# Kernel optimization log

Hardware: AMD Instinct MI355X
Metric: run time of the kernel (lower is better)

The kernel has to match this reference:

```python
import jax, jax.numpy as jnp
import numpy as np

B, T, E, H = 64, 512, 256, 128


def setup_inputs() -> dict:
    key = jax.random.key(0)
    ks = jax.random.split(key, 7)
    s = 1.0 / np.sqrt(H)  # PyTorch LSTM default init range
    inputs = jax.random.normal(ks[0], (B, T, E), jnp.float32)
    labels = jax.random.randint(ks[1], (B, T), 0, H)
    W_ih = jax.random.uniform(ks[2], (4 * H, E), jnp.float32, -s, s)
    W_hh = jax.random.uniform(ks[3], (4 * H, H), jnp.float32, -s, s)
    b_ih = jax.random.uniform(ks[4], (4 * H,), jnp.float32, -s, s)
    b_hh = jax.random.uniform(ks[5], (4 * H,), jnp.float32, -s, s)
    transition = jax.random.uniform(ks[6], (H, H), jnp.float32)  # torch.rand
    return {"inputs": inputs, "labels": labels, "W_ih": W_ih, "W_hh": W_hh,
            "b_ih": b_ih, "b_hh": b_hh, "transition": transition}


def _lstm(x, W_ih, W_hh, b_ih, b_hh):
    # x: (T, B, E) -> hs: (T, B, H). PyTorch gate order: i, f, g, o.
    Bn = x.shape[1]
    Hn = W_hh.shape[1]

    def step(carry, xt):
        h, c = carry
        g = xt @ W_ih.T + b_ih + h @ W_hh.T + b_hh  # (B, 4H)
        i, f, gg, o = jnp.split(g, 4, axis=-1)
        c = jax.nn.sigmoid(f) * c + jax.nn.sigmoid(i) * jnp.tanh(gg)
        h = jax.nn.sigmoid(o) * jnp.tanh(c)
        return (h, c), h

    h0 = jnp.zeros((Bn, Hn), x.dtype)
    (_, _), hs = jax.lax.scan(step, (h0, h0), x)
    return hs


def reference(inputs, labels, W_ih, W_hh, b_ih, b_hh, transition):
    x = inputs.transpose(1, 0, 2)  # (T, B, E)
    trans = jax.nn.softmax(transition, axis=1)  # row-softmax transition
    hs = _lstm(x, W_ih, W_hh, b_ih, b_hh)  # (T, B, H)
    Hbth = jax.nn.softmax(hs, axis=2).transpose(1, 0, 2)  # (B, T, H)

    # gold-path score Pr: emissions at gold tags + transition scores
    emit = jnp.take_along_axis(Hbth, labels[:, :, None], axis=2)[..., 0].sum(axis=1)  # (B,)
    tr_score = trans[labels[:, :-1], labels[:, 1:]].sum(axis=1)  # (B,)
    Pr = emit + tr_score

    # CRF forward algorithm (partition score Ps) via scan over time
    pre0 = Hbth[:, 0, :] + trans[0]  # (B, H)

    def crf_step(pre, h_t):
        # Z[b, i, j] = pre[b, i] + trans[i, j] + h_t[b, j]
        Z = pre[:, :, None] + trans[None] + h_t[:, None, :]
        return jax.nn.logsumexp(Z, axis=1), None

    pre, _ = jax.lax.scan(crf_step, pre0, Hbth[:, 1:, :].transpose(1, 0, 2))
    Ps = jax.nn.logsumexp(pre + trans[-1][None, :], axis=1)  # (B,)

    return (Ps - Pr).sum()
```

## Files before the change

### kernel.cpp

```cpp
#include <hip/hip_runtime.h>
#include <hip/hip_bf16.h>
#include <cstdint>

#define BB 64
#define TT 512
#define EE 256
#define HH 128
#define G4 512

typedef _Float16 half2_t __attribute__((ext_vector_type(2)));
typedef _Float16 f16x4 __attribute__((ext_vector_type(4)));
typedef _Float16 f16x8 __attribute__((ext_vector_type(8)));
typedef float f32x4 __attribute__((ext_vector_type(4)));

#define BC(x) __builtin_bit_cast(half2_t, x)

__device__ __forceinline__ float fdot2f(half2_t a, half2_t b, float c) {
#if defined(__has_builtin)
#if __has_builtin(__builtin_amdgcn_fdot2)
  return __builtin_amdgcn_fdot2(a, b, c, false);
#else
  return c + (float)a[0] * (float)b[0] + (float)a[1] * (float)b[1];
#endif
#else
  return c + (float)a[0] * (float)b[0] + (float)a[1] * (float)b[1];
#endif
}

__device__ __forceinline__ float rcp_(float x) { return __builtin_amdgcn_rcpf(x); }
__device__ __forceinline__ float tanh_(float x) {
  float ax = fabsf(x);
  float e = __expf(-2.f * ax);
  float r = (1.f - e) * rcp_(1.f + e);
  return copysignf(r, x);
}

__device__ __forceinline__ float readlane_f(float x, int lane) {
#if defined(__has_builtin)
#if __has_builtin(__builtin_amdgcn_readlane)
  return __builtin_bit_cast(float, __builtin_amdgcn_readlane(__builtin_bit_cast(int, x), lane));
#else
  return __shfl(x, lane);
#endif
#else
  return __shfl(x, lane);
#endif
}

#if defined(__has_builtin)
#if __has_builtin(__builtin_amdgcn_update_dpp)
#define HAVE_DPP 1
#endif
#endif

__device__ __forceinline__ float wave_sum64_bcast(float x) {
#ifdef HAVE_DPP
#define DPP_ADD(ctrl)                                                          \
  {                                                                            \
    int _t = __builtin_amdgcn_update_dpp(0, __builtin_bit_cast(int, x), ctrl,  \
                                         0xf, 0xf, true);                      \
    x += __builtin_bit_cast(float, _t);                                        \
  }
  DPP_ADD(0x111)
  DPP_ADD(0x112)
  DPP_ADD(0x114)
  DPP_ADD(0x118)
  DPP_ADD(0x142)
  DPP_ADD(0x143)
#undef DPP_ADD
  return readlane_f(x, 63);
#else
#pragma unroll
  for (int s = 1; s <= 32; s <<= 1) x += __shfl_xor(x, s);
  return x;
#endif
}

__global__ __launch_bounds__(128) void prep_kernel(
    const float* __restrict__ transition, const float* __restrict__ W_ih,
    float* __restrict__ trans, _Float16* __restrict__ W16) {
  const int bid = blockIdx.x, t = threadIdx.x;
  if (bid < 128) {
    __shared__ float red[2];
    float v = transition[bid * HH + t];
    float m = v;
#pragma unroll
    for (int s = 32; s >= 1; s >>= 1) m = fmaxf(m, __shfl_xor(m, s));
    if ((t & 63) == 0) red[t >> 6] = m;
    __syncthreads();
    m = fmaxf(red[0], red[1]);
    float e = __expf(v - m);
    float s = e;
#pragma unroll
    for (int k = 32; k >= 1; k >>= 1) s += __shfl_xor(s, k);
    __syncthreads();
    if ((t & 63) == 0) red[t >> 6] = s;
    __syncthreads();
    trans[bid * HH + t] = e * rcp_(red[0] + red[1]);
  } else {
    const int base = (bid - 128) * 1024 + t * 8;
    float4 v0 = *(const float4*)(W_ih + base);
    float4 v1 = *(const float4*)(W_ih + base + 4);
    f16x8 h;
    h[0] = (_Float16)v0.x; h[1] = (_Float16)v0.y;
    h[2] = (_Float16)v0.z; h[3] = (_Float16)v0.w;
    h[4] = (_Float16)v1.x; h[5] = (_Float16)v1.y;
    h[6] = (_Float16)v1.z; h[7] = (_Float16)v1.w;
    *(f16x8*)(W16 + base) = h;
  }
}

__global__ __launch_bounds__(256) void gemm_in(
    const float* __restrict__ A, const _Float16* __restrict__ W16,
    const float* __restrict__ b_ih, const float* __restrict__ b_hh,
    float* __restrict__ out) {
  __shared__ _Float16 As[64][264];
  const int t = threadIdx.x;
  const int m0 = blockIdx.x * 64;
  const int n0 = blockIdx.y * 256;
  {
    const int c4 = t & 63, r0 = t >> 6;
#pragma unroll
    for (int p = 0; p < 16; ++p) {
      const int row = r0 + 4 * p;
      float4 v = *(const float4*)(A + (size_t)(m0 + row) * EE + c4 * 4);
      f16x4 h;
      h[0] = (_Float16)v.x; h[1] = (_Float16)v.y;
      h[2] = (_Float16)v.z; h[3] = (_Float16)v.w;
      *(f16x4*)&As[row][c4 * 4] = h;
    }
  }
  __syncthreads();
  const int w = t >> 6, L = t & 63;
  const int lrow = L & 15, quad = L >> 4, lk = quad * 8;
  f32x4 acc[4][4] = {};
  const _Float16* Wbase = W16 + (size_t)(n0 + w * 64) * EE;
#pragma unroll
  for (int kc = 0; kc < 8; ++kc) {
    f16x8 a[4], bf[4];
#pragma unroll
    for (int mf = 0; mf < 4; ++mf)
      a[mf] = *(const f16x8*)&As[mf * 16 + lrow][kc * 32 + lk];
#pragma unroll
    for (int nf = 0; nf < 4; ++nf)
      bf[nf] = *(const f16x8*)(Wbase + (size_t)(nf * 16 + lrow) * EE + kc * 32 + lk);
#pragma unroll
    for (int mf = 0; mf < 4; ++mf)
#pragma unroll
      for (int nf = 0; nf < 4; ++nf)
        acc[mf][nf] = __builtin_amdgcn_mfma_f32_16x16x32_f16(a[mf], bf[nf], acc[mf][nf], 0, 0, 0);
  }
#pragma unroll
  for (int nf = 0; nf < 4; ++nf) {
    const int j = n0 + w * 64 + nf * 16 + lrow;
    const float bias = b_ih[j] + b_hh[j];
#pragma unroll
    for (int mf = 0; mf < 4; ++mf) {
#pragma unroll
      for (int r = 0; r < 4; ++r) {
        const int m = m0 + mf * 16 + quad * 4 + r;
        out[(size_t)m * G4 + j] = acc[mf][nf][r] + bias;
      }
    }
  }
}

__global__ __launch_bounds__(512, 2) void lstm_crf(
    const float* __restrict__ precomp, const float* __restrict__ Whh,
    const float* __restrict__ trans, const int* __restrict__ labels,
    float* __restrict__ out_b) {
  const int b = blockIdx.x, t = threadIdx.x;
  const int g = t >> 7;
  const int j = t & 127;

  __shared__ __align__(16) _Float16 h_lds[HH];
  __shared__ __align__(16) _Float16 E_lds[HH];
  __shared__ __align__(16) float act2[G4];
  __shared__ __align__(16) float Spart2[G4];
  __shared__ int lab[TT];

  half2_t w[64];
  {
    const float4* wr = (const float4*)(Whh + (size_t)t * HH);
#pragma unroll
    for (int i = 0; i < 32; ++i) {
      float4 v = wr[i];
      half2_t p0, p1;
      p0[0] = (_Float16)v.x; p0[1] = (_Float16)v.y;
      p1[0] = (_Float16)v.z; p1[1] = (_Float16)v.w;
      w[2 * i] = p0; w[2 * i + 1] = p1;
    }
  }
  half2_t et[16];
#pragma unroll
  for (int a = 0; a < 16; ++a) {
    float e0 = __expf(trans[(g * 32 + 2 * a) * HH + j]);
    float e1 = __expf(trans[(g * 32 + 2 * a + 1) * HH + j]);
    half2_t h2; h2[0] = (_Float16)e0; h2[1] = (_Float16)e1;
    et[a] = h2;
  }
  lab[t] = labels[b * TT + t];
  if (t < HH) { h_lds[t] = (_Float16)0.f; E_lds[t] = (_Float16)0.f; }

  float tr0x = 0.f, tr0y = 0.f, tr127x = 0.f, tr127y = 0.f;
  if (t < 64) {
    float2 v0 = *(const float2*)(trans + 2 * t);
    float2 v1 = *(const float2*)(trans + 127 * HH + 2 * t);
    tr0x = v0.x; tr0y = v0.y; tr127x = v1.x; tr127y = v1.y;
  }
  float c0 = 0.f, c1 = 0.f, preA = 0.f, preB = 0.f, mused = 0.f, emit = 0.f;

  const float* pcb = precomp + (size_t)b * TT * G4 + t;
  float cbuf[8], nbuf[8];
#pragma unroll
  for (int k = 0; k < 8; ++k) cbuf[k] = pcb[(size_t)k * G4];
  __syncthreads();

#pragma unroll 1
  for (int base = 0; base < TT; base += 8) {
    const bool more = (base + 8 < TT);
    if (more) {
#pragma unroll
      for (int k = 0; k < 8; ++k) nbuf[k] = pcb[(size_t)(base + 8 + k) * G4];
    }
#pragma unroll
    for (int k = 0; k < 8; ++k) {
      const int step = base + k;
      const float cur = cbuf[k];
      float a0 = 0.f, a1 = 0.f, a2 = 0.f, a3 = 0.f;
      const float4* hv4 = (const float4*)h_lds;
#pragma unroll
      for (int kc = 0; kc < 16; ++kc) {
        float4 hb = hv4[kc];
        a0 = fdot2f(w[4 * kc + 0], BC(hb.x), a0);
        a1 = fdot2f(w[4 * kc + 1], BC(hb.y), a1);
        a2 = fdot2f(w[4 * kc + 2], BC(hb.z), a2);
        a3 = fdot2f(w[4 * kc + 3], BC(hb.w), a3);
      }
      float s0 = 0.f, s1 = 0.f;
      const float4* ev4 = (const float4*)E_lds + g * 4;
#pragma unroll
      for (int ec = 0; ec < 4; ++ec) {
        float4 eb = ev4[ec];
        s0 = fdot2f(et[4 * ec + 0], BC(eb.x), s0);
        s1 = fdot2f(et[4 * ec + 1], BC(eb.y), s1);
        s0 = fdot2f(et[4 * ec + 2], BC(eb.z), s0);
        s1 = fdot2f(et[4 * ec + 3], BC(eb.w), s1);
      }
      const float gate = cur + ((a0 + a1) + (a2 + a3));
      const bool isg = (g == 2);
      const float yy = isg ? (-2.f * fabsf(gate)) : (-gate);
      const float exv = __expf(yy);
      const float num = isg ? (1.f - exv) : 1.f;
      float av = num * rcp_(1.f + exv);
      av = isg ? copysignf(av, gate) : av;
      act2[j * 4 + g] = av;
      Spart2[j * 4 + g] = s0 + s1;
      __syncthreads();
      if (t < 64) {
        const float4* av4 = (const float4*)act2;
        float4 A0 = av4[2 * t], A1 = av4[2 * t + 1];
        const float4* sv4 = (const float4*)Spart2;
        float4 S0v = sv4[2 * t], S1v = sv4[2 * t + 1];
        c0 = A0.y * c0 + A0.x * A0.z;
        c1 = A1.y * c1 + A1.x * A1.z;
        const float h0 = A0.w * tanh_(c0), h1 = A1.w * tanh_(c1);
        const float e0 = __expf(h0), e1 = __expf(h1);
        const float denom = wave_sum64_bcast(e0 + e1);
        const float rinv = rcp_(denom);
        const float p0 = e0 * rinv, p1 = e1 * rinv;
        const float Sa = (S0v.x + S0v.y) + (S0v.z + S0v.w);
        const float Sb = (S1v.x + S1v.y) + (S1v.z + S1v.w);
        const float lgSa = __logf(Sa), lgSb = __logf(Sb);
        const float lgS0 = readlane_f(lgSa, 0);
        const int lb = lab[step];
        const float Mnext = (step == 0) ? 0.f : (mused + lgS0);
        preA = p0 + ((step == 0) ? tr0x : (mused + lgSa));
        preB = p1 + ((step == 0) ? tr0y : (mused + lgSb));
        if (2 * t == lb) emit += p0;
        if (2 * t + 1 == lb) emit += p1;
        half2_t Eh;
        Eh[0] = (_Float16)__expf(preA - Mnext);
        Eh[1] = (_Float16)__expf(preB - Mnext);
        *(half2_t*)&E_lds[2 * t] = Eh;
        half2_t Hh;
        Hh[0] = (_Float16)h0; Hh[1] = (_Float16)h1;
        *(half2_t*)&h_lds[2 * t] = Hh;
        mused = Mnext;
      }
      __syncthreads();
    }
    if (more) {
#pragma unroll
      for (int k = 0; k < 8; ++k) cbuf[k] = nbuf[k];
    }
  }
  if (t < 64) {
    float v0 = preA + tr127x, v1 = preB + tr127y;
    float m = fmaxf(v0, v1);
#pragma unroll
    for (int s = 1; s <= 32; s <<= 1) m = fmaxf(m, __shfl_xor(m, s));
    float ex = __expf(v0 - m) + __expf(v1 - m);
    float em = emit;
#pragma unroll
    for (int s = 1; s <= 32; s <<= 1) {
      ex += __shfl_xor(ex, s);
      em += __shfl_xor(em, s);
    }
    if (t == 0) out_b[b] = m + __logf(ex) - em;
  }
}

__global__ __launch_bounds__(512) void finalize_kernel(
    const float* __restrict__ trans, const int* __restrict__ labels,
    const float* __restrict__ out_b, float* __restrict__ d_out) {
  const int t = threadIdx.x;
  float a = 0.f;
  if (t < TT - 1) {
    for (int b = 0; b < BB; ++b) {
      const int l0 = labels[b * TT + t];
      const int l1 = labels[b * TT + t + 1];
      a += trans[l0 * HH + l1];
    }
  }
  float x = ((t < BB) ? out_b[t] : 0.f) - a;
  __shared__ float red[8];
#pragma unroll
  for (int s = 32; s >= 1; s >>= 1) x += __shfl_xor(x, s);
  if ((t & 63) == 0) red[t >> 6] = x;
  __syncthreads();
  if (t == 0) {
    float s = 0.f;
#pragma unroll
    for (int i = 0; i < 8; ++i) s += red[i];
    d_out[0] = s;
  }
}

extern "C" void kernel_launch(void* const* d_in, const int* in_sizes, int n_in,
                              void* d_out, int out_size, void* d_ws, size_t ws_size,
                              hipStream_t stream) {
  const float* inputs = (const float*)d_in[0];
  const int* labels = (const int*)d_in[1];
  const float* W_ih = (const float*)d_in[2];
  const float* W_hh = (const float*)d_in[3];
  const float* b_ih = (const float*)d_in[4];
  const float* b_hh = (const float*)d_in[5];
  const float* transition = (const float*)d_in[6];

  char* ws = (char*)d_ws;
  float* precomp = (float*)ws;
  float* trans = (float*)(ws + 67108864);
  _Float16* W16 = (_Float16*)(ws + 67108864 + 65536);
  float* out_b = (float*)(ws + 67108864 + 65536 + 262144);

  prep_kernel<<<256, 128, 0, stream>>>(transition, W_ih, trans, W16);
  gemm_in<<<dim3(512, 2), 256, 0, stream>>>(inputs, W16, b_ih, b_hh, precomp);
  lstm_crf<<<64, 512, 0, stream>>>(precomp, W_hh, trans, labels, out_b);
  finalize_kernel<<<1, 512, 0, stream>>>(trans, labels, out_b, (float*)d_out);
}
```

Before: 605.5 us.

## Halve recurrent block to 256 threads, each computing two gate rows

The sequential LSTM+CRF kernel now launches 256 threads per batch element instead of 512. Each thread holds two W_hh rows and two transition column slices in registers and computes two gates per step. Gate rows t and t+256 pair a sigmoid gate with either the tanh (g) gate or the o gate, and the act/Spart LDS layout changes to match. The aim is to make each per-step __syncthreads barrier cheaper with fewer waves, at the cost of doubling per-thread register use and serial ALU work per step.

New measurement: 620.8 us. +2.5%, slower.

```diff
diff --git a/kernel.cpp b/kernel.cpp
--- a/kernel.cpp
+++ b/kernel.cpp
@@ -165,41 +165,52 @@
   }
 }
 
-__global__ __launch_bounds__(512, 2) void lstm_crf(
+__global__ __launch_bounds__(256) void lstm_crf(
     const float* __restrict__ precomp, const float* __restrict__ Whh,
     const float* __restrict__ trans, const int* __restrict__ labels,
     float* __restrict__ out_b) {
   const int b = blockIdx.x, t = threadIdx.x;
-  const int g = t >> 7;
+  const int g0 = t >> 7;
   const int j = t & 127;
 
   __shared__ __align__(16) _Float16 h_lds[HH];
   __shared__ __align__(16) _Float16 E_lds[HH];
-  __shared__ __align__(16) float act2[G4];
-  __shared__ __align__(16) float Spart2[G4];
+  __shared__ __align__(16) float act[G4];
+  __shared__ __align__(16) float Spart[G4];
   __shared__ int lab[TT];
 
-  half2_t w[64];
+  half2_t w0[64], w1[64];
   {
-    const float4* wr = (const float4*)(Whh + (size_t)t * HH);
+    const float4* wr0 = (const float4*)(Whh + (size_t)t * HH);
+    const float4* wr1 = (const float4*)(Whh + (size_t)(t + 256) * HH);
 #pragma unroll
     for (int i = 0; i < 32; ++i) {
-      float4 v = wr[i];
+      float4 v = wr0[i];
       half2_t p0, p1;
       p0[0] = (_Float16)v.x; p0[1] = (_Float16)v.y;
       p1[0] = (_Float16)v.z; p1[1] = (_Float16)v.w;
-      w[2 * i] = p0; w[2 * i + 1] = p1;
-    }
-  }
-  half2_t et[16];
+      w0[2 * i] = p0; w0[2 * i + 1] = p1;
+      float4 u = wr1[i];
+      half2_t q0, q1;
+      q0[0] = (_Float16)u.x; q0[1] = (_Float16)u.y;
+      q1[0] = (_Float16)u.z; q1[1] = (_Float16)u.w;
+      w1[2 * i] = q0; w1[2 * i + 1] = q1;
+    }
+  }
+  half2_t et0[16], et1[16];
 #pragma unroll
   for (int a = 0; a < 16; ++a) {
-    float e0 = __expf(trans[(g * 32 + 2 * a) * HH + j]);
-    float e1 = __expf(trans[(g * 32 + 2 * a + 1) * HH + j]);
+    float e0 = __expf(trans[(g0 * 32 + 2 * a) * HH + j]);
+    float e1 = __expf(trans[(g0 * 32 + 2 * a + 1) * HH + j]);
     half2_t h2; h2[0] = (_Float16)e0; h2[1] = (_Float16)e1;
-    et[a] = h2;
+    et0[a] = h2;
+    float f0 = __expf(trans[((g0 + 2) * 32 + 2 * a) * HH + j]);
+    float f1 = __expf(trans[((g0 + 2) * 32 + 2 * a + 1) * HH + j]);
+    half2_t h3; h3[0] = (_Float16)f0; h3[1] = (_Float16)f1;
+    et1[a] = h3;
   }
   lab[t] = labels[b * TT + t];
+  lab[t + 256] = labels[b * TT + t + 256];
   if (t < HH) { h_lds[t] = (_Float16)0.f; E_lds[t] = (_Float16)0.f; }
 
   float tr0x = 0.f, tr0y = 0.f, tr127x = 0.f, tr127y = 0.f;
@@ -210,10 +221,14 @@
   }
   float c0 = 0.f, c1 = 0.f, preA = 0.f, preB = 0.f, mused = 0.f, emit = 0.f;
 
-  const float* pcb = precomp + (size_t)b * TT * G4 + t;
-  float cbuf[8], nbuf[8];
-#pragma unroll
-  for (int k = 0; k < 8; ++k) cbuf[k] = pcb[(size_t)k * G4];
+  const float* pc0 = precomp + (size_t)b * TT * G4 + t;
+  const float* pc1 = pc0 + 256;
+  float cb0[8], cb1[8], nb0[8], nb1[8];
+#pragma unroll
+  for (int k = 0; k < 8; ++k) {
+    cb0[k] = pc0[(size_t)k * G4];
+    cb1[k] = pc1[(size_t)k * G4];
+  }
   __syncthreads();
 
 #pragma unroll 1
@@ -221,56 +236,73 @@
     const bool more = (base + 8 < TT);
     if (more) {
 #pragma unroll
-      for (int k = 0; k < 8; ++k) nbuf[k] = pcb[(size_t)(base + 8 + k) * G4];
+      for (int k = 0; k < 8; ++k) {
+        nb0[k] = pc0[(size_t)(base + 8 + k) * G4];
+        nb1[k] = pc1[(size_t)(base + 8 + k) * G4];
+      }
     }
 #pragma unroll
     for (int k = 0; k < 8; ++k) {
       const int step = base + k;
-      const float cur = cbuf[k];
-      float a0 = 0.f, a1 = 0.f, a2 = 0.f, a3 = 0.f;
+      float a00 = 0.f, a01 = 0.f, a10 = 0.f, a11 = 0.f;
       const float4* hv4 = (const float4*)h_lds;
 #pragma unroll
       for (int kc = 0; kc < 16; ++kc) {
         float4 hb = hv4[kc];
-        a0 = fdot2f(w[4 * kc + 0], BC(hb.x), a0);
-        a1 = fdot2f(w[4 * kc + 1], BC(hb.y), a1);
-        a2 = fdot2f(w[4 * kc + 2], BC(hb.z), a2);
-        a3 = fdot2f(w[4 * kc + 3], BC(hb.w), a3);
-      }
-      float s0 = 0.f, s1 = 0.f;
-      const float4* ev4 = (const float4*)E_lds + g * 4;
+        const half2_t hx = BC(hb.x), hy = BC(hb.y), hz = BC(hb.z), hw = BC(hb.w);
+        a00 = fdot2f(w0[4 * kc + 0], hx, a00);
+        a01 = fdot2f(w0[4 * kc + 1], hy, a01);
+        a00 = fdot2f(w0[4 * kc + 2], hz, a00);
+        a01 = fdot2f(w0[4 * kc + 3], hw, a01);
+        a10 = fdot2f(w1[4 * kc + 0], hx, a10);
+        a11 = fdot2f(w1[4 * kc + 1], hy, a11);
+        a10 = fdot2f(w1[4 * kc + 2], hz, a10);
+        a11 = fdot2f(w1[4 * kc + 3], hw, a11);
+      }
+      float s00 = 0.f, s01 = 0.f, s10 = 0.f, s11 = 0.f;
+      const float4* e0v = (const float4*)E_lds + g0 * 4;
+      const float4* e1v = (const float4*)E_lds + (g0 + 2) * 4;
 #pragma unroll
       for (int ec = 0; ec < 4; ++ec) {
-        float4 eb = ev4[ec];
-        s0 = fdot2f(et[4 * ec + 0], BC(eb.x), s0);
-        s1 = fdot2f(et[4 * ec + 1], BC(eb.y), s1);
-        s0 = fdot2f(et[4 * ec + 2], BC(eb.z), s0);
-        s1 = fdot2f(et[4 * ec + 3], BC(eb.w), s1);
-      }
-      const float gate = cur + ((a0 + a1) + (a2 + a3));
-      const bool isg = (g == 2);
-      const float yy = isg ? (-2.f * fabsf(gate)) : (-gate);
+        float4 ea = e0v[ec];
+        s00 = fdot2f(et0[4 * ec + 0], BC(ea.x), s00);
+        s01 = fdot2f(et0[4 * ec + 1], BC(ea.y), s01);
+        s00 = fdot2f(et0[4 * ec + 2], BC(ea.z), s00);
+        s01 = fdot2f(et0[4 * ec + 3], BC(ea.w), s01);
+        float4 eb = e1v[ec];
+        s10 = fdot2f(et1[4 * ec + 0], BC(eb.x), s10);
+        s11 = fdot2f(et1[4 * ec + 1], BC(eb.y), s11);
+        s10 = fdot2f(et1[4 * ec + 2], BC(eb.z), s10);
+        s11 = fdot2f(et1[4 * ec + 3], BC(eb.w), s11);
+      }
+      const float gate0 = cb0[k] + (a00 + a01);
+      const float gate1 = cb1[k] + (a10 + a11);
+      const float av0 = rcp_(1.f + __expf(-gate0));
+      const bool isg = (g0 == 0);
+      const float yy = isg ? (-2.f * fabsf(gate1)) : (-gate1);
       const float exv = __expf(yy);
       const float num = isg ? (1.f - exv) : 1.f;
-      float av = num * rcp_(1.f + exv);
-      av = isg ? copysignf(av, gate) : av;
-      act2[j * 4 + g] = av;
-      Spart2[j * 4 + g] = s0 + s1;
+      float av1 = num * rcp_(1.f + exv);
+      av1 = isg ? copysignf(av1, gate1) : av1;
+      act[t] = av0;
+      act[t + 256] = av1;
+      Spart[t] = s00 + s01;
+      Spart[t + 256] = s10 + s11;
       __syncthreads();
       if (t < 64) {
-        const float4* av4 = (const float4*)act2;
-        float4 A0 = av4[2 * t], A1 = av4[2 * t + 1];
-        const float4* sv4 = (const float4*)Spart2;
-        float4 S0v = sv4[2 * t], S1v = sv4[2 * t + 1];
-        c0 = A0.y * c0 + A0.x * A0.z;
-        c1 = A1.y * c1 + A1.x * A1.z;
-        const float h0 = A0.w * tanh_(c0), h1 = A1.w * tanh_(c1);
+        const float2* a2 = (const float2*)act;
+        float2 I = a2[t], F = a2[64 + t], G = a2[128 + t], O = a2[192 + t];
+        const float2* s2 = (const float2*)Spart;
+        float2 Sq0 = s2[t], Sq1 = s2[64 + t], Sq2 = s2[128 + t], Sq3 = s2[192 + t];
+        c0 = F.x * c0 + I.x * G.x;
+        c1 = F.y * c1 + I.y * G.y;
+        const float h0 = O.x * tanh_(c0), h1 = O.y * tanh_(c1);
         const float e0 = __expf(h0), e1 = __expf(h1);
         const float denom = wave_sum64_bcast(e0 + e1);
         const float rinv = rcp_(denom);
         const float p0 = e0 * rinv, p1 = e1 * rinv;
-        const float Sa = (S0v.x + S0v.y) + (S0v.z + S0v.w);
-        const float Sb = (S1v.x + S1v.y) + (S1v.z + S1v.w);
+        const float Sa = (Sq0.x + Sq1.x) + (Sq2.x + Sq3.x);
+        const float Sb = (Sq0.y + Sq1.y) + (Sq2.y + Sq3.y);
         const float lgSa = __logf(Sa), lgSb = __logf(Sb);
         const float lgS0 = readlane_f(lgSa, 0);
         const int lb = lab[step];
@@ -292,7 +324,7 @@
     }
     if (more) {
 #pragma unroll
-      for (int k = 0; k < 8; ++k) cbuf[k] = nbuf[k];
+      for (int k = 0; k < 8; ++k) { cb0[k] = nb0[k]; cb1[k] = nb1[k]; }
     }
   }
   if (t < 64) {
@@ -356,6 +388,6 @@
 
   prep_kernel<<<256, 128, 0, stream>>>(transition, W_ih, trans, W16);
   gemm_in<<<dim3(512, 2), 256, 0, stream>>>(inputs, W16, b_ih, b_hh, precomp);
-  lstm_crf<<<64, 512, 0, stream>>>(precomp, W_hh, trans, labels, out_b);
+  lstm_crf<<<64, 256, 0, stream>>>(precomp, W_hh, trans, labels, out_b);
   finalize_kernel<<<1, 512, 0, stream>>>(trans, labels, out_b, (float*)d_out);
 }
```

## Pack two batch sequences per 1024-thread block in LSTM-CRF kernel

Applied to the files above, without the earlier changes.

Each block now processes two batch elements, with one 512-thread half per sequence, halving the grid to 32 blocks. The gate and partition LDS buffers change from an interleaved j*4+g layout to a gate-major layout read as float2. The apparent aim is to share barriers and the CU across two independent recurrences to hide latency. The 1024-thread launch bound limits registers per thread, so the per-thread weight arrays may spill. Half as many CUs are used.

Result: slower. 1.158 ms (+91.2%).

```diff
diff --git a/kernel.cpp b/kernel.cpp
--- a/kernel.cpp
+++ b/kernel.cpp
@@ -165,23 +165,26 @@
   }
 }
 
-__global__ __launch_bounds__(512, 2) void lstm_crf(
+__global__ __launch_bounds__(1024) void lstm_crf(
     const float* __restrict__ precomp, const float* __restrict__ Whh,
     const float* __restrict__ trans, const int* __restrict__ labels,
     float* __restrict__ out_b) {
-  const int b = blockIdx.x, t = threadIdx.x;
-  const int g = t >> 7;
-  const int j = t & 127;
-
-  __shared__ __align__(16) _Float16 h_lds[HH];
-  __shared__ __align__(16) _Float16 E_lds[HH];
-  __shared__ __align__(16) float act2[G4];
-  __shared__ __align__(16) float Spart2[G4];
-  __shared__ int lab[TT];
+  const int t = threadIdx.x;
+  const int cc = t >> 9;
+  const int tt = t & 511;
+  const int bb = blockIdx.x * 2 + cc;
+  const int g = tt >> 7;
+  const int j = tt & 127;
+
+  __shared__ __align__(16) _Float16 h_lds[2][HH];
+  __shared__ __align__(16) _Float16 E_lds[2][HH];
+  __shared__ __align__(16) float act[2][G4];
+  __shared__ __align__(16) float Spart[2][G4];
+  __shared__ int lab[2][TT];
 
   half2_t w[64];
   {
-    const float4* wr = (const float4*)(Whh + (size_t)t * HH);
+    const float4* wr = (const float4*)(Whh + (size_t)tt * HH);
 #pragma unroll
     for (int i = 0; i < 32; ++i) {
       float4 v = wr[i];
@@ -199,18 +202,18 @@
     half2_t h2; h2[0] = (_Float16)e0; h2[1] = (_Float16)e1;
     et[a] = h2;
   }
-  lab[t] = labels[b * TT + t];
-  if (t < HH) { h_lds[t] = (_Float16)0.f; E_lds[t] = (_Float16)0.f; }
+  lab[cc][tt] = labels[bb * TT + tt];
+  if (tt < HH) { h_lds[cc][tt] = (_Float16)0.f; E_lds[cc][tt] = (_Float16)0.f; }
 
   float tr0x = 0.f, tr0y = 0.f, tr127x = 0.f, tr127y = 0.f;
-  if (t < 64) {
-    float2 v0 = *(const float2*)(trans + 2 * t);
-    float2 v1 = *(const float2*)(trans + 127 * HH + 2 * t);
+  if (tt < 64) {
+    float2 v0 = *(const float2*)(trans + 2 * tt);
+    float2 v1 = *(const float2*)(trans + 127 * HH + 2 * tt);
     tr0x = v0.x; tr0y = v0.y; tr127x = v1.x; tr127y = v1.y;
   }
   float c0 = 0.f, c1 = 0.f, preA = 0.f, preB = 0.f, mused = 0.f, emit = 0.f;
 
-  const float* pcb = precomp + (size_t)b * TT * G4 + t;
+  const float* pcb = precomp + (size_t)bb * TT * G4 + tt;
   float cbuf[8], nbuf[8];
 #pragma unroll
   for (int k = 0; k < 8; ++k) cbuf[k] = pcb[(size_t)k * G4];
@@ -228,7 +231,7 @@
       const int step = base + k;
       const float cur = cbuf[k];
       float a0 = 0.f, a1 = 0.f, a2 = 0.f, a3 = 0.f;
-      const float4* hv4 = (const float4*)h_lds;
+      const float4* hv4 = (const float4*)h_lds[cc];
 #pragma unroll
       for (int kc = 0; kc < 16; ++kc) {
         float4 hb = hv4[kc];
@@ -238,7 +241,7 @@
         a3 = fdot2f(w[4 * kc + 3], BC(hb.w), a3);
       }
       float s0 = 0.f, s1 = 0.f;
-      const float4* ev4 = (const float4*)E_lds + g * 4;
+      const float4* ev4 = (const float4*)E_lds[cc] + g * 4;
 #pragma unroll
       for (int ec = 0; ec < 4; ++ec) {
         float4 eb = ev4[ec];
@@ -254,38 +257,38 @@
       const float num = isg ? (1.f - exv) : 1.f;
       float av = num * rcp_(1.f + exv);
       av = isg ? copysignf(av, gate) : av;
-      act2[j * 4 + g] = av;
-      Spart2[j * 4 + g] = s0 + s1;
+      act[cc][tt] = av;
+      Spart[cc][tt] = s0 + s1;
       __syncthreads();
-      if (t < 64) {
-        const float4* av4 = (const float4*)act2;
-        float4 A0 = av4[2 * t], A1 = av4[2 * t + 1];
-        const float4* sv4 = (const float4*)Spart2;
-        float4 S0v = sv4[2 * t], S1v = sv4[2 * t + 1];
-        c0 = A0.y * c0 + A0.x * A0.z;
-        c1 = A1.y * c1 + A1.x * A1.z;
-        const float h0 = A0.w * tanh_(c0), h1 = A1.w * tanh_(c1);
+      if (tt < 64) {
+        const float2* a2p = (const float2*)act[cc];
+        float2 I = a2p[tt], F = a2p[64 + tt], G = a2p[128 + tt], O = a2p[192 + tt];
+        const float2* s2p = (const float2*)Spart[cc];
+        float2 Sq0 = s2p[tt], Sq1 = s2p[64 + tt], Sq2 = s2p[128 + tt], Sq3 = s2p[192 + tt];
+        c0 = F.x * c0 + I.x * G.x;
+        c1 = F.y * c1 + I.y * G.y;
+        const float h0 = O.x * tanh_(c0), h1 = O.y * tanh_(c1);
         const float e0 = __expf(h0), e1 = __expf(h1);
         const float denom = wave_sum64_bcast(e0 + e1);
         const float rinv = rcp_(denom);
         const float p0 = e0 * rinv, p1 = e1 * rinv;
-        const float Sa = (S0v.x + S0v.y) + (S0v.z + S0v.w);
-        const float Sb = (S1v.x + S1v.y) + (S1v.z + S1v.w);
+        const float Sa = (Sq0.x + Sq1.x) + (Sq2.x + Sq3.x);
+        const float Sb = (Sq0.y + Sq1.y) + (Sq2.y + Sq3.y);
         const float lgSa = __logf(Sa), lgSb = __logf(Sb);
         const float lgS0 = readlane_f(lgSa, 0);
-        const int lb = lab[step];
+        const int lb = lab[cc][step];
         const float Mnext = (step == 0) ? 0.f : (mused + lgS0);
         preA = p0 + ((step == 0) ? tr0x : (mused + lgSa));
         preB = p1 + ((step == 0) ? tr0y : (mused + lgSb));
-        if (2 * t == lb) emit += p0;
-        if (2 * t + 1 == lb) emit += p1;
+        if (2 * tt == lb) emit += p0;
+        if (2 * tt + 1 == lb) emit += p1;
         half2_t Eh;
         Eh[0] = (_Float16)__expf(preA - Mnext);
         Eh[1] = (_Float16)__expf(preB - Mnext);
-        *(half2_t*)&E_lds[2 * t] = Eh;
+        *(half2_t*)&E_lds[cc][2 * tt] = Eh;
         half2_t Hh;
         Hh[0] = (_Float16)h0; Hh[1] = (_Float16)h1;
-        *(half2_t*)&h_lds[2 * t] = Hh;
+        *(half2_t*)&h_lds[cc][2 * tt] = Hh;
         mused = Mnext;
       }
       __syncthreads();
@@ -295,7 +298,7 @@
       for (int k = 0; k < 8; ++k) cbuf[k] = nbuf[k];
     }
   }
-  if (t < 64) {
+  if (tt < 64) {
     float v0 = preA + tr127x, v1 = preB + tr127y;
     float m = fmaxf(v0, v1);
 #pragma unroll
@@ -307,7 +310,7 @@
       ex += __shfl_xor(ex, s);
       em += __shfl_xor(em, s);
     }
-    if (t == 0) out_b[b] = m + __logf(ex) - em;
+    if (tt == 0) out_b[bb] = m + __logf(ex) - em;
   }
 }
 
@@ -356,6 +359,6 @@
 
   prep_kernel<<<256, 128, 0, stream>>>(transition, W_ih, trans, W16);
   gemm_in<<<dim3(512, 2), 256, 0, stream>>>(inputs, W16, b_ih, b_hh, precomp);
-  lstm_crf<<<64, 512, 0, stream>>>(precomp, W_hh, trans, labels, out_b);
+  lstm_crf<<<32, 1024, 0, stream>>>(precomp, W_hh, trans, labels, out_b);
   finalize_kernel<<<1, 512, 0, stream>>>(trans, labels, out_b, (float*)d_out);
 }
```

## Use MFMA for LSTM recurrent matvec with gate-interleaved weight layout

Applied to the files above, without the earlier changes.

Replaces the per-thread fdot2 recurrent matvec with 16x16x32 f16 MFMA instructions. W_hh and the precomputed input projection are permuted so the four gates of each hidden unit sit in adjacent columns, which lets the cell update be done inside the MFMA wave without the act2 LDS round-trip. The h buffer is double-buffered, barriers use a custom lgkmcnt wait, and the precomp prefetch now covers one step instead of eight. This is meant to shorten the serial per-step latency, but the matvec computes redundant columns and the launch bound drops to one block per CU.

New measurement: 579.3 us. 4.3% less time.

```diff
diff --git a/kernel.cpp b/kernel.cpp
--- a/kernel.cpp
+++ b/kernel.cpp
@@ -15,6 +15,8 @@
 
 #define BC(x) __builtin_bit_cast(half2_t, x)
 
+#define BAR() asm volatile("s_waitcnt lgkmcnt(0)\n\ts_barrier" ::: "memory")
+
 __device__ __forceinline__ float fdot2f(half2_t a, half2_t b, float c) {
 #if defined(__has_builtin)
 #if __has_builtin(__builtin_amdgcn_fdot2)
@@ -28,6 +30,7 @@
 }
 
 __device__ __forceinline__ float rcp_(float x) { return __builtin_amdgcn_rcpf(x); }
+__device__ __forceinline__ float sigmoid_(float x) { return rcp_(1.f + __expf(-x)); }
 __device__ __forceinline__ float tanh_(float x) {
   float ax = fabsf(x);
   float e = __expf(-2.f * ax);
@@ -76,6 +79,10 @@
 #endif
 }
 
+__device__ __host__ __forceinline__ int permj(int j) {
+  return ((j & 127) << 2) | (j >> 7);
+}
+
 __global__ __launch_bounds__(128) void prep_kernel(
     const float* __restrict__ transition, const float* __restrict__ W_ih,
     float* __restrict__ trans, _Float16* __restrict__ W16) {
@@ -99,6 +106,8 @@
     trans[bid * HH + t] = e * rcp_(red[0] + red[1]);
   } else {
     const int base = (bid - 128) * 1024 + t * 8;
+    const int row = base >> 8;
+    const int col = base & 255;
     float4 v0 = *(const float4*)(W_ih + base);
     float4 v1 = *(const float4*)(W_ih + base + 4);
     f16x8 h;
@@ -106,7 +115,7 @@
     h[2] = (_Float16)v0.z; h[3] = (_Float16)v0.w;
     h[4] = (_Float16)v1.x; h[5] = (_Float16)v1.y;
     h[6] = (_Float16)v1.z; h[7] = (_Float16)v1.w;
-    *(f16x8*)(W16 + base) = h;
+    *(f16x8*)(W16 + (size_t)permj(row) * EE + col) = h;
   }
 }
 
@@ -153,7 +162,8 @@
 #pragma unroll
   for (int nf = 0; nf < 4; ++nf) {
     const int j = n0 + w * 64 + nf * 16 + lrow;
-    const float bias = b_ih[j] + b_hh[j];
+    const int jo = ((j & 3) << 7) | (j >> 2);
+    const float bias = b_ih[jo] + b_hh[jo];
 #pragma unroll
     for (int mf = 0; mf < 4; ++mf) {
 #pragma unroll
@@ -165,42 +175,49 @@
   }
 }
 
-__global__ __launch_bounds__(512, 2) void lstm_crf(
+__global__ __launch_bounds__(512, 1) void lstm_crf(
     const float* __restrict__ precomp, const float* __restrict__ Whh,
     const float* __restrict__ trans, const int* __restrict__ labels,
     float* __restrict__ out_b) {
   const int b = blockIdx.x, t = threadIdx.x;
-  const int g = t >> 7;
-  const int j = t & 127;
-
-  __shared__ __align__(16) _Float16 h_lds[HH];
+  const int w = t >> 6, l = t & 63, q = l >> 4, l15 = l & 15;
+  const int c2 = l15 & 3;
+  const int g2 = t >> 7, jj = t & 127;
+
+  __shared__ __align__(16) _Float16 h_lds[2][HH];
   __shared__ __align__(16) _Float16 E_lds[HH];
-  __shared__ __align__(16) float act2[G4];
-  __shared__ __align__(16) float Spart2[G4];
+  __shared__ __align__(16) float Spart[G4];
   __shared__ int lab[TT];
 
-  half2_t w[64];
-  {
-    const float4* wr = (const float4*)(Whh + (size_t)t * HH);
-#pragma unroll
-    for (int i = 0; i < 32; ++i) {
-      float4 v = wr[i];
-      half2_t p0, p1;
-      p0[0] = (_Float16)v.x; p0[1] = (_Float16)v.y;
-      p1[0] = (_Float16)v.z; p1[1] = (_Float16)v.w;
-      w[2 * i] = p0; w[2 * i + 1] = p1;
+  f16x8 wfr[4][4];
+#pragma unroll
+  for (int tf = 0; tf < 4; ++tf) {
+    const int rowp = 16 * (4 * w + tf) + l15;
+    const int u = rowp >> 2, g = rowp & 3;
+    const float* src = Whh + (size_t)(g * HH + u) * HH;
+#pragma unroll
+    for (int kt = 0; kt < 4; ++kt) {
+      const float* s8 = src + kt * 32 + q * 8;
+      float4 v0 = *(const float4*)s8;
+      float4 v1 = *(const float4*)(s8 + 4);
+      f16x8 h8;
+      h8[0] = (_Float16)v0.x; h8[1] = (_Float16)v0.y;
+      h8[2] = (_Float16)v0.z; h8[3] = (_Float16)v0.w;
+      h8[4] = (_Float16)v1.x; h8[5] = (_Float16)v1.y;
+      h8[6] = (_Float16)v1.z; h8[7] = (_Float16)v1.w;
+      wfr[tf][kt] = h8;
     }
   }
   half2_t et[16];
 #pragma unroll
   for (int a = 0; a < 16; ++a) {
-    float e0 = __expf(trans[(g * 32 + 2 * a) * HH + j]);
-    float e1 = __expf(trans[(g * 32 + 2 * a + 1) * HH + j]);
+    float e0 = __expf(trans[(g2 * 32 + 2 * a) * HH + jj]);
+    float e1 = __expf(trans[(g2 * 32 + 2 * a + 1) * HH + jj]);
     half2_t h2; h2[0] = (_Float16)e0; h2[1] = (_Float16)e1;
     et[a] = h2;
   }
   lab[t] = labels[b * TT + t];
-  if (t < HH) { h_lds[t] = (_Float16)0.f; E_lds[t] = (_Float16)0.f; }
+  if (t < HH) { h_lds[0][t] = (_Float16)0.f; E_lds[t] = (_Float16)0.f; }
 
   float tr0x = 0.f, tr0y = 0.f, tr127x = 0.f, tr127y = 0.f;
   if (t < 64) {
@@ -208,92 +225,91 @@
     float2 v1 = *(const float2*)(trans + 127 * HH + 2 * t);
     tr0x = v0.x; tr0y = v0.y; tr127x = v1.x; tr127y = v1.y;
   }
-  float c0 = 0.f, c1 = 0.f, preA = 0.f, preB = 0.f, mused = 0.f, emit = 0.f;
-
-  const float* pcb = precomp + (size_t)b * TT * G4 + t;
-  float cbuf[8], nbuf[8];
-#pragma unroll
-  for (int k = 0; k < 8; ++k) cbuf[k] = pcb[(size_t)k * G4];
+  float cst = 0.f;
+  float preA = 0.f, preB = 0.f, mused = 0.f, emit = 0.f;
+
+  const float* pcb = precomp + (size_t)b * TT * G4 + 64 * w + 4 * q;
+  f32x4 pc_cur[4], pc_nxt[4];
+#pragma unroll
+  for (int tf = 0; tf < 4; ++tf) pc_cur[tf] = *(const f32x4*)(pcb + 16 * tf);
   __syncthreads();
 
 #pragma unroll 1
-  for (int base = 0; base < TT; base += 8) {
-    const bool more = (base + 8 < TT);
-    if (more) {
-#pragma unroll
-      for (int k = 0; k < 8; ++k) nbuf[k] = pcb[(size_t)(base + 8 + k) * G4];
-    }
-#pragma unroll
-    for (int k = 0; k < 8; ++k) {
-      const int step = base + k;
-      const float cur = cbuf[k];
-      float a0 = 0.f, a1 = 0.f, a2 = 0.f, a3 = 0.f;
-      const float4* hv4 = (const float4*)h_lds;
-#pragma unroll
-      for (int kc = 0; kc < 16; ++kc) {
-        float4 hb = hv4[kc];
-        a0 = fdot2f(w[4 * kc + 0], BC(hb.x), a0);
-        a1 = fdot2f(w[4 * kc + 1], BC(hb.y), a1);
-        a2 = fdot2f(w[4 * kc + 2], BC(hb.z), a2);
-        a3 = fdot2f(w[4 * kc + 3], BC(hb.w), a3);
-      }
-      float s0 = 0.f, s1 = 0.f;
-      const float4* ev4 = (const float4*)E_lds + g * 4;
-#pragma unroll
-      for (int ec = 0; ec < 4; ++ec) {
-        float4 eb = ev4[ec];
-        s0 = fdot2f(et[4 * ec + 0], BC(eb.x), s0);
-        s1 = fdot2f(et[4 * ec + 1], BC(eb.y), s1);
-        s0 = fdot2f(et[4 * ec + 2], BC(eb.z), s0);
-        s1 = fdot2f(et[4 * ec + 3], BC(eb.w), s1);
-      }
-      const float gate = cur + ((a0 + a1) + (a2 + a3));
-      const bool isg = (g == 2);
-      const float yy = isg ? (-2.f * fabsf(gate)) : (-gate);
-      const float exv = __expf(yy);
-      const float num = isg ? (1.f - exv) : 1.f;
-      float av = num * rcp_(1.f + exv);
-      av = isg ? copysignf(av, gate) : av;
-      act2[j * 4 + g] = av;
-      Spart2[j * 4 + g] = s0 + s1;
-      __syncthreads();
-      if (t < 64) {
-        const float4* av4 = (const float4*)act2;
-        float4 A0 = av4[2 * t], A1 = av4[2 * t + 1];
-        const float4* sv4 = (const float4*)Spart2;
-        float4 S0v = sv4[2 * t], S1v = sv4[2 * t + 1];
-        c0 = A0.y * c0 + A0.x * A0.z;
-        c1 = A1.y * c1 + A1.x * A1.z;
-        const float h0 = A0.w * tanh_(c0), h1 = A1.w * tanh_(c1);
-        const float e0 = __expf(h0), e1 = __expf(h1);
-        const float denom = wave_sum64_bcast(e0 + e1);
-        const float rinv = rcp_(denom);
-        const float p0 = e0 * rinv, p1 = e1 * rinv;
-        const float Sa = (S0v.x + S0v.y) + (S0v.z + S0v.w);
-        const float Sb = (S1v.x + S1v.y) + (S1v.z + S1v.w);
-        const float lgSa = __logf(Sa), lgSb = __logf(Sb);
-        const float lgS0 = readlane_f(lgSa, 0);
-        const int lb = lab[step];
-        const float Mnext = (step == 0) ? 0.f : (mused + lgS0);
-        preA = p0 + ((step == 0) ? tr0x : (mused + lgSa));
-        preB = p1 + ((step == 0) ? tr0y : (mused + lgSb));
-        if (2 * t == lb) emit += p0;
-        if (2 * t + 1 == lb) emit += p1;
-        half2_t Eh;
-        Eh[0] = (_Float16)__expf(preA - Mnext);
-        Eh[1] = (_Float16)__expf(preB - Mnext);
-        *(half2_t*)&E_lds[2 * t] = Eh;
-        half2_t Hh;
-        Hh[0] = (_Float16)h0; Hh[1] = (_Float16)h1;
-        *(half2_t*)&h_lds[2 * t] = Hh;
-        mused = Mnext;
-      }
-      __syncthreads();
-    }
-    if (more) {
-#pragma unroll
-      for (int k = 0; k < 8; ++k) cbuf[k] = nbuf[k];
-    }
+  for (int step = 0; step < TT; ++step) {
+    const int pr = step & 1;
+    const int sn = (step < TT - 1) ? step + 1 : step;
+#pragma unroll
+    for (int tf = 0; tf < 4; ++tf)
+      pc_nxt[tf] = *(const f32x4*)(pcb + (size_t)sn * G4 + 16 * tf);
+    const f16x8 hb0 = *(const f16x8*)&h_lds[pr][q * 8];
+    const f16x8 hb1 = *(const f16x8*)&h_lds[pr][32 + q * 8];
+    const f16x8 hb2 = *(const f16x8*)&h_lds[pr][64 + q * 8];
+    const f16x8 hb3 = *(const f16x8*)&h_lds[pr][96 + q * 8];
+    f32x4 a0 = pc_cur[0], a1 = pc_cur[1], a2 = pc_cur[2], a3 = pc_cur[3];
+    a0 = __builtin_amdgcn_mfma_f32_16x16x32_f16(wfr[0][0], hb0, a0, 0, 0, 0);
+    a1 = __builtin_amdgcn_mfma_f32_16x16x32_f16(wfr[1][0], hb0, a1, 0, 0, 0);
+    a2 = __builtin_amdgcn_mfma_f32_16x16x32_f16(wfr[2][0], hb0, a2, 0, 0, 0);
+    a3 = __builtin_amdgcn_mfma_f32_16x16x32_f16(wfr[3][0], hb0, a3, 0, 0, 0);
+    a0 = __builtin_amdgcn_mfma_f32_16x16x32_f16(wfr[0][1], hb1, a0, 0, 0, 0);
+    a1 = __builtin_amdgcn_mfma_f32_16x16x32_f16(wfr[1][1], hb1, a1, 0, 0, 0);
+    a2 = __builtin_amdgcn_mfma_f32_16x16x32_f16(wfr[2][1], hb1, a2, 0, 0, 0);
+    a3 = __builtin_amdgcn_mfma_f32_16x16x32_f16(wfr[3][1], hb1, a3, 0, 0, 0);
+    a0 = __builtin_amdgcn_mfma_f32_16x16x32_f16(wfr[0][2], hb2, a0, 0, 0, 0);
+    a1 = __builtin_amdgcn_mfma_f32_16x16x32_f16(wfr[1][2], hb2, a1, 0, 0, 0);
+    a2 = __builtin_amdgcn_mfma_f32_16x16x32_f16(wfr[2][2], hb2, a2, 0, 0, 0);
+    a3 = __builtin_amdgcn_mfma_f32_16x16x32_f16(wfr[3][2], hb2, a3, 0, 0, 0);
+    a0 = __builtin_amdgcn_mfma_f32_16x16x32_f16(wfr[0][3], hb3, a0, 0, 0, 0);
+    a1 = __builtin_amdgcn_mfma_f32_16x16x32_f16(wfr[1][3], hb3, a1, 0, 0, 0);
+    a2 = __builtin_amdgcn_mfma_f32_16x16x32_f16(wfr[2][3], hb3, a2, 0, 0, 0);
+    a3 = __builtin_amdgcn_mfma_f32_16x16x32_f16(wfr[3][3], hb3, a3, 0, 0, 0);
+    float s0 = 0.f, s1 = 0.f;
+    const float4* ev4 = (const float4*)E_lds + g2 * 4;
+#pragma unroll
+    for (int ec = 0; ec < 4; ++ec) {
+      float4 eb = ev4[ec];
+      s0 = fdot2f(et[4 * ec + 0], BC(eb.x), s0);
+      s1 = fdot2f(et[4 * ec + 1], BC(eb.y), s1);
+      s0 = fdot2f(et[4 * ec + 2], BC(eb.z), s0);
+      s1 = fdot2f(et[4 * ec + 3], BC(eb.w), s1);
+    }
+    const f32x4 ac = (c2 == 0) ? a0 : (c2 == 1) ? a1 : (c2 == 2) ? a2 : a3;
+    const float iv = sigmoid_(ac[0]);
+    const float fv = sigmoid_(ac[1]);
+    const float gv = tanh_(ac[2]);
+    const float ov = sigmoid_(ac[3]);
+    cst = fv * cst + iv * gv;
+    const float hv = ov * tanh_(cst);
+    if (l15 < 4) h_lds[pr ^ 1][16 * w + 4 * l15 + q] = (_Float16)hv;
+    Spart[t] = s0 + s1;
+    BAR();
+    if (t < 64) {
+      const half2_t hp = *(const half2_t*)&h_lds[pr ^ 1][2 * t];
+      const float h0 = (float)hp[0], h1 = (float)hp[1];
+      const float e0 = __expf(h0), e1 = __expf(h1);
+      const float denom = wave_sum64_bcast(e0 + e1);
+      const float rinv = rcp_(denom);
+      const float p0 = e0 * rinv, p1 = e1 * rinv;
+      const float2* s2p = (const float2*)Spart;
+      float2 Sq0 = s2p[t], Sq1 = s2p[64 + t], Sq2 = s2p[128 + t], Sq3 = s2p[192 + t];
+      const float Sa = (Sq0.x + Sq1.x) + (Sq2.x + Sq3.x);
+      const float Sb = (Sq0.y + Sq1.y) + (Sq2.y + Sq3.y);
+      const float lgSa = __logf(Sa), lgSb = __logf(Sb);
+      const float lgS0 = readlane_f(lgSa, 0);
+      const int lb = lab[step];
+      const float Mnext = (step == 0) ? 0.f : (mused + lgS0);
+      preA = p0 + ((step == 0) ? tr0x : (mused + lgSa));
+      preB = p1 + ((step == 0) ? tr0y : (mused + lgSb));
+      if (2 * t == lb) emit += p0;
+      if (2 * t + 1 == lb) emit += p1;
+      half2_t Eh;
+      Eh[0] = (_Float16)__expf(preA - Mnext);
+      Eh[1] = (_Float16)__expf(preB - Mnext);
+      *(half2_t*)&E_lds[2 * t] = Eh;
+      mused = Mnext;
+    }
+    BAR();
+#pragma unroll
+    for (int tf = 0; tf < 4; ++tf) pc_cur[tf] = pc_nxt[tf];
   }
   if (t < 64) {
     float v0 = preA + tr127x, v1 = preB + tr127y;
```
